# Kernel tuning notes

Measured on AMD Instinct MI355X. Metric: run time of the kernel, lower is better.

Reference implementation:

```python
import jax, jax.numpy as jnp
import numpy as np

B, S, H = 8, 2048, 1024

def setup_inputs() -> dict:
    key = jax.random.key(0)
    ks = jax.random.split(key, 7)
    s = 1.0 / np.sqrt(H)
    return {
        "x": jax.random.normal(ks[0], (B, S, H), dtype=jnp.float32),
        "Wq": jax.random.normal(ks[1], (H, H), dtype=jnp.float32) * s,
        "bq": jnp.zeros((H,), dtype=jnp.float32),
        "Wk": jax.random.normal(ks[2], (H, H), dtype=jnp.float32) * s,
        "bk": jnp.zeros((H,), dtype=jnp.float32),
        "Wv": jax.random.normal(ks[3], (H, H), dtype=jnp.float32) * s,
        "bv": jnp.zeros((H,), dtype=jnp.float32),
    }

def reference(x, Wq, bq, Wk, bk, Wv, bv):
    # Q,K,V: [B,S,H]
    Q = x @ Wq + bq
    K = x @ Wk + bk
    V = x @ Wv + bv
    scale = 1.0 / jnp.sqrt(jnp.asarray(K.shape[-1], dtype=Q.dtype))
    scores = jnp.einsum("bqh,bkh->bqk", Q, K) * scale  # [B,S,S]
    attn = jax.nn.softmax(scores, axis=-1)
    return jnp.einsum("bqk,bkh->bqh", attn, V)
```

## Files before the change

### kernel.cpp

```cpp
#include <hip/hip_runtime.h>
#include <stdint.h>

#define BD 8
#define SD 2048
#define HD 1024

typedef __bf16 bf16x8 __attribute__((ext_vector_type(8)));
typedef float f32x4 __attribute__((ext_vector_type(4)));
typedef unsigned short u16x8 __attribute__((ext_vector_type(8)));
typedef unsigned short u16x4 __attribute__((ext_vector_type(4)));

typedef const __attribute__((address_space(1))) void* gas_ptr;
typedef __attribute__((address_space(3))) void* las_ptr;

__device__ __forceinline__ void gload16(const void* g, void* l) {
  __builtin_amdgcn_global_load_lds((gas_ptr)g, (las_ptr)l, 16, 0, 0);
}

__device__ __forceinline__ unsigned short f32_to_bf16(float f) {
  union { float f; unsigned u; } v; v.f = f;
  unsigned u = v.u;
  return (unsigned short)((u + 0x7FFFu + ((u >> 16) & 1u)) >> 16);
}
__device__ __forceinline__ float bf16_to_f32(unsigned short h) {
  union { unsigned u; float f; } v; v.u = ((unsigned)h) << 16;
  return v.f;
}

__global__ __launch_bounds__(256) void cast_x_kernel(
    const float* __restrict__ x, unsigned short* __restrict__ xb) {
  size_t i = (size_t)blockIdx.x * 256 + threadIdx.x;
  const float4* xp = (const float4*)x;
  float4 a = xp[2*i], b = xp[2*i + 1];
  float v[8] = {a.x,a.y,a.z,a.w,b.x,b.y,b.z,b.w};
  u16x8 o;
#pragma unroll
  for (int j = 0; j < 8; j++) o[j] = f32_to_bf16(v[j]);
  *(u16x8*)(xb + i*8) = o;
}

__global__ __launch_bounds__(256) void transpose_w_kernel(
    const float* __restrict__ Wq, const float* __restrict__ Wk,
    const float* __restrict__ Wv, unsigned short* __restrict__ wt) {
  __shared__ float tile[32][33];
  const int w = blockIdx.z;
  const float* W = (w == 0) ? Wq : ((w == 1) ? Wk : Wv);
  const int n0 = blockIdx.x * 32, k0 = blockIdx.y * 32;
  const int x = threadIdx.x, y = threadIdx.y;
  for (int j = 0; j < 32; j += 8)
    tile[y + j][x] = W[(size_t)(k0 + y + j) * HD + n0 + x];
  __syncthreads();
  unsigned short* dst = wt + (size_t)w * HD * HD;
  for (int j = 0; j < 32; j += 8)
    dst[(size_t)(n0 + y + j) * HD + k0 + x] = f32_to_bf16(tile[x][y + j]);
}

template<int OUT_MODE>
__global__ __launch_bounds__(512, 2) void gemm256(
    const unsigned short* __restrict__ A, size_t sA,
    const unsigned short* __restrict__ Bt, size_t sB,
    const float* __restrict__ b0, const float* __restrict__ b1,
    const float* __restrict__ b2,
    float* __restrict__ Cf, unsigned short* __restrict__ Cb, size_t sC,
    int M, int N, int K, float alpha)
{
  __shared__ unsigned short As[2 * 256 * 64];
  __shared__ unsigned short Bs[2 * 256 * 64];

  const int gx = gridDim.x, gy = gridDim.y;
  const int nwg = gx * gy * gridDim.z;
  const int flat = blockIdx.x + gx * (blockIdx.y + gy * blockIdx.z);
  const int swz = (flat & 7) * (nwg >> 3) + (flat >> 3);
  const int tz = swz / (gx * gy);
  const int rem = swz - tz * gx * gy;
  const int ty = rem / gx, tx = rem - (rem / gx) * gx;
  const int m0 = ty * 256, n0 = tx * 256;

  A  += (size_t)tz * sA;
  Bt += (size_t)tz * sB;
  const float* bias = (tz == 0) ? b0 : ((tz == 1) ? b1 : b2);

  const int tid = threadIdx.x, lane = tid & 63, w = tid >> 6;
  const int wr = w >> 2, wc = w & 3;
  const int nt = K >> 6;

  const int lrow = lane >> 3;
  const int sslot8 = (((lane & 7) ^ ((lane >> 3) & 7)) << 3);

  const int rA = wr * 128 + (lane & 15);
  const int rB = wc * 64 + (lane & 15);
  const int qq = lane >> 4;
  const int sxor = lane & 7;

#define STAGE_A(t,h) do { \
    const unsigned short* _g = A + (size_t)(m0 + (h)*128 + w*16 + lrow) * K + (size_t)((t)*64 + sslot8); \
    unsigned short* _l = &As[((((t)&1)*256 + (h)*128 + w*16)) * 64]; \
    gload16(_g, _l); gload16(_g + (size_t)8*K, _l + 512); } while(0)
#define STAGE_B(t,h) do { \
    const unsigned short* _g = Bt + (size_t)(n0 + (h)*128 + w*16 + lrow) * K + (size_t)((t)*64 + sslot8); \
    unsigned short* _l = &Bs[((((t)&1)*256 + (h)*128 + w*16)) * 64]; \
    gload16(_g, _l); gload16(_g + (size_t)8*K, _l + 512); } while(0)
#define LDA(buf,m,ks) __builtin_bit_cast(bf16x8, *(const u16x8*)(&As[(buf)*16384 + (rA + (m)*16)*64 + ((((ks)*4 + qq) ^ sxor) << 3)]))
#define LDB(buf,n,ks) __builtin_bit_cast(bf16x8, *(const u16x8*)(&Bs[(buf)*16384 + (rB + (n)*16)*64 + ((((ks)*4 + qq) ^ sxor) << 3)]))
#define MFMA_Q(AV,MBASE,NLO) \
    _Pragma("unroll") for (int _m = 0; _m < 4; _m++) \
    _Pragma("unroll") for (int _n = 0; _n < 2; _n++) \
    _Pragma("unroll") for (int _k = 0; _k < 2; _k++) \
      acc[(MBASE)+_m][(NLO)+_n] = __builtin_amdgcn_mfma_f32_16x16x32_bf16( \
          AV[_m][_k], bv[(NLO)+_n][_k], acc[(MBASE)+_m][(NLO)+_n], 0, 0, 0);

  f32x4 acc[8][4] = {};
  bf16x8 av0[4][2], av1[4][2], bv[4][2];

  STAGE_B(0,0); STAGE_B(0,1); STAGE_A(0,0); STAGE_A(0,1);
  STAGE_B(1,0); STAGE_B(1,1); STAGE_A(1,0);
  asm volatile("s_waitcnt vmcnt(6)" ::: "memory");
  __builtin_amdgcn_s_barrier();

  for (int t = 0; t < nt; ++t) {
    const int cur = t & 1;
#pragma unroll
    for (int n = 0; n < 4; n++) { bv[n][0] = LDB(cur,n,0); bv[n][1] = LDB(cur,n,1); }
#pragma unroll
    for (int m = 0; m < 4; m++) { av0[m][0] = LDA(cur,m,0); av0[m][1] = LDA(cur,m,1); }
    if (t + 1 < nt) STAGE_A(t+1, 1);
    __builtin_amdgcn_s_barrier();
    __builtin_amdgcn_s_setprio(1);
    MFMA_Q(av0, 0, 0);
    __builtin_amdgcn_s_setprio(0);
    __builtin_amdgcn_s_barrier();
#pragma unroll
    for (int m = 0; m < 4; m++) { av1[m][0] = LDA(cur,m+4,0); av1[m][1] = LDA(cur,m+4,1); }
    if (t + 2 < nt) STAGE_B(t+2, 0);
    __builtin_amdgcn_s_barrier();
    __builtin_amdgcn_s_setprio(1);
    MFMA_Q(av0, 0, 2);
    __builtin_amdgcn_s_setprio(0);
    __builtin_amdgcn_s_barrier();
    if (t + 2 < nt) STAGE_B(t+2, 1);
    __builtin_amdgcn_s_barrier();
    __builtin_amdgcn_s_setprio(1);
    MFMA_Q(av1, 4, 0);
    __builtin_amdgcn_s_setprio(0);
    __builtin_amdgcn_s_barrier();
    if (t + 2 < nt) STAGE_A(t+2, 0);
    __builtin_amdgcn_s_barrier();
    __builtin_amdgcn_s_setprio(1);
    MFMA_Q(av1, 4, 2);
    __builtin_amdgcn_s_setprio(0);
    if (t < nt - 2) asm volatile("s_waitcnt vmcnt(6)" ::: "memory");
    else            asm volatile("s_waitcnt vmcnt(0)" ::: "memory");
    __builtin_amdgcn_s_barrier();
  }

  const bool transposed = (OUT_MODE == 2) && (tz == 2);
  if (OUT_MODE == 0) {
    float* Cfz = Cf + (size_t)tz * sC;
#pragma unroll
    for (int n = 0; n < 4; n++) {
      const int col = n0 + wc * 64 + n * 16 + (lane & 15);
      const float bvv = bias ? bias[col] : 0.0f;
#pragma unroll
      for (int m = 0; m < 8; m++) {
        const int row = m0 + wr * 128 + m * 16 + (lane >> 4) * 4;
#pragma unroll
        for (int r = 0; r < 4; r++)
          Cfz[(size_t)(row + r) * N + col] = (acc[m][n][r] + bvv) * alpha;
      }
    }
  } else if (!transposed) {
    unsigned short* Cbz = Cb + (size_t)tz * sC;
    unsigned short* base = (w < 4) ? (As + w * 8192) : (Bs + (w - 4) * 8192);
    float bvv[4];
#pragma unroll
    for (int n = 0; n < 4; n++)
      bvv[n] = bias ? bias[n0 + wc * 64 + n * 16 + (lane & 15)] : 0.0f;
#pragma unroll
    for (int n = 0; n < 4; n++)
#pragma unroll
      for (int m = 0; m < 8; m++)
#pragma unroll
        for (int r = 0; r < 4; r++) {
          const int lr = m * 16 + (lane >> 4) * 4 + r;
          const int lc = n * 16 + (lane & 15);
          base[lr * 64 + ((((lc >> 3) ^ (lr & 7)) << 3) | (lc & 7))] =
              f32_to_bf16((acc[m][n][r] + bvv[n]) * alpha);
        }
#pragma unroll
    for (int i = 0; i < 16; i++) {
      const int lr = i * 8 + (lane >> 3);
      u16x8 vrow = *(const u16x8*)(base + lr * 64 + (((lane & 7) ^ (lr & 7)) << 3));
      *(u16x8*)(Cbz + (size_t)(m0 + wr * 128 + lr) * N
                + (n0 + wc * 64 + (lane & 7) * 8)) = vrow;
    }
  } else {
    unsigned short* Vt = Cb + (size_t)2 * sC;
    unsigned short* Vtb = Vt + (size_t)(m0 >> 11) * (HD * SD);
    const int s0 = (m0 & 2047) + wr * 128;
    const int h0 = n0 + wc * 64;
    unsigned short* base = (w < 4) ? (As + w * 8192) : (Bs + (w - 4) * 8192);
    float bvv[4];
#pragma unroll
    for (int n = 0; n < 4; n++)
      bvv[n] = bias ? bias[h0 + n * 16 + (lane & 15)] : 0.0f;
#pragma unroll
    for (int n = 0; n < 4; n++) {
      const int col = n * 16 + (lane & 15);
      const int x = (col & 7) << 3;
#pragma unroll
      for (int m = 0; m < 8; m++) {
        const int row0 = m * 16 + (lane >> 4) * 4;
        u16x4 pk;
#pragma unroll
        for (int r = 0; r < 4; r++)
          pk[r] = f32_to_bf16((acc[m][n][r] + bvv[n]) * alpha);
        *(u16x4*)(base + col * 128 + (row0 ^ x)) = pk;
      }
    }
#pragma unroll
    for (int i = 0; i < 16; i++) {
      const int c = i * 4 + (lane >> 4);
      const int j = lane & 15;
      u16x8 vrow = *(const u16x8*)(base + c * 128 + ((j * 8) ^ ((c & 7) << 3)));
      *(u16x8*)(Vtb + (size_t)(h0 + c) * SD + s0 + j * 8) = vrow;
    }
  }
#undef STAGE_A
#undef STAGE_B
#undef LDA
#undef LDB
#undef MFMA_Q
}

__global__ __launch_bounds__(256) void softmax_bf16_kernel(
    unsigned short* __restrict__ S) {
  const int row = blockIdx.x;
  unsigned short* sp = S + (size_t)row * SD;
  const int tid = threadIdx.x, lane = tid & 63, w = tid >> 6;
  u16x8 raw = *(const u16x8*)(sp + tid * 8);
  float x[8];
#pragma unroll
  for (int j = 0; j < 8; j++) x[j] = bf16_to_f32(raw[j]);
  float m = x[0];
#pragma unroll
  for (int j = 1; j < 8; j++) m = fmaxf(m, x[j]);
#pragma unroll
  for (int off = 32; off >= 1; off >>= 1) m = fmaxf(m, __shfl_xor(m, off));
  __shared__ float redm[4];
  if (lane == 0) redm[w] = m;
  __syncthreads();
  m = fmaxf(fmaxf(redm[0], redm[1]), fmaxf(redm[2], redm[3]));
  float e[8]; float s = 0.0f;
#pragma unroll
  for (int j = 0; j < 8; j++) { e[j] = __expf(x[j] - m); s += e[j]; }
#pragma unroll
  for (int off = 32; off >= 1; off >>= 1) s += __shfl_xor(s, off);
  __shared__ float reds[4];
  if (lane == 0) reds[w] = s;
  __syncthreads();
  s = reds[0] + reds[1] + reds[2] + reds[3];
  const float inv = 1.0f / s;
  u16x8 o;
#pragma unroll
  for (int j = 0; j < 8; j++) o[j] = f32_to_bf16(e[j] * inv);
  *(u16x8*)(sp + tid * 8) = o;
}

extern "C" void kernel_launch(void* const* d_in, const int* in_sizes, int n_in,
                              void* d_out, int out_size, void* d_ws, size_t ws_size,
                              hipStream_t stream) {
  const float* x  = (const float*)d_in[0];
  const float* Wq = (const float*)d_in[1];
  const float* bq = (const float*)d_in[2];
  const float* Wk = (const float*)d_in[3];
  const float* bk = (const float*)d_in[4];
  const float* Wv = (const float*)d_in[5];
  const float* bv = (const float*)d_in[6];
  float* out = (float*)d_out;
  char* ws = (char*)d_ws;
  const size_t MB = 1024 * 1024;
  const float scale = 0.03125f;
  const size_t BH = (size_t)SD * HD;
  const size_t SS = (size_t)SD * SD;

  unsigned short* wt = (unsigned short*)(ws + 0);
  unsigned short* Qb = (unsigned short*)(ws + 6 * MB);
  unsigned short* Kb = (unsigned short*)(ws + 38 * MB);
  unsigned short* Vt = (unsigned short*)(ws + 70 * MB);
  unsigned short* xb = (unsigned short*)(ws + 102 * MB);
  unsigned short* Pb = (unsigned short*)(ws + 102 * MB);

  int G;
  if      (ws_size >= 166 * MB) G = 8;
  else if (ws_size >= 134 * MB) G = 4;
  else if (ws_size >= 118 * MB) G = 2;
  else                          G = 1;

  transpose_w_kernel<<<dim3(32, 32, 3), dim3(32, 8), 0, stream>>>(Wq, Wk, Wv, wt);
  cast_x_kernel<<<8192, 256, 0, stream>>>(x, xb);

  gemm256<2><<<dim3(HD/256, (BD*SD)/256, 3), 512, 0, stream>>>(
      xb, 0, wt, (size_t)HD*HD, bq, bk, bv,
      nullptr, Qb, (size_t)16*MB, BD*SD, HD, HD, 1.0f);

  const int ngroups = BD / G;
  for (int g = 0; g < ngroups; g++) {
    gemm256<1><<<dim3(SD/256, SD/256, G), 512, 0, stream>>>(
        Qb + (size_t)g*G*BH, BH, Kb + (size_t)g*G*BH, BH,
        nullptr, nullptr, nullptr, nullptr, Pb, SS, SD, SD, HD, scale);
    softmax_bf16_kernel<<<G*SD, 256, 0, stream>>>(Pb);
    gemm256<0><<<dim3(HD/256, SD/256, G), 512, 0, stream>>>(
        Pb, SS, Vt + (size_t)g*G*BH, BH, nullptr, nullptr, nullptr,
        out + (size_t)g*G*BH, nullptr, BH, SD, HD, SD, 1.0f);
  }
}
```

Before: 295.1 us.

## Fuse fp32-to-bf16 cast of x into QKV projection GEMM A-tile staging

Removes the separate cast_x kernel and its bf16 intermediate buffer. The QKV GEMM now loads fp32 x directly through registers, converts it to bf16 and writes it into swizzled LDS, while B still uses async global-to-LDS loads. This saves one kernel launch and a write and read of the bf16 copy of x. In exchange, fp32 A reads are re-done by each of the 12 N/z tiles (4 N tiles times Q, K and V), doubling A-read bytes per tile. The synchronous register staging with lgkmcnt waits may also hurt the GEMM pipeline's overlap.

```diff
diff --git a/kernel.cpp b/kernel.cpp
--- a/kernel.cpp
+++ b/kernel.cpp
@@ -25,18 +25,6 @@
 __device__ __forceinline__ float bf16_to_f32(unsigned short h) {
   union { unsigned u; float f; } v; v.u = ((unsigned)h) << 16;
   return v.f;
-}
-
-__global__ __launch_bounds__(256) void cast_x_kernel(
-    const float* __restrict__ x, unsigned short* __restrict__ xb) {
-  size_t i = (size_t)blockIdx.x * 256 + threadIdx.x;
-  const float4* xp = (const float4*)x;
-  float4 a = xp[2*i], b = xp[2*i + 1];
-  float v[8] = {a.x,a.y,a.z,a.w,b.x,b.y,b.z,b.w};
-  u16x8 o;
-#pragma unroll
-  for (int j = 0; j < 8; j++) o[j] = f32_to_bf16(v[j]);
-  *(u16x8*)(xb + i*8) = o;
 }
 
 __global__ __launch_bounds__(256) void transpose_w_kernel(
@@ -55,9 +43,10 @@
     dst[(size_t)(n0 + y + j) * HD + k0 + x] = f32_to_bf16(tile[x][y + j]);
 }
 
-template<int OUT_MODE>
+template<int OUT_MODE, int A_F32>
 __global__ __launch_bounds__(512, 2) void gemm256(
     const unsigned short* __restrict__ A, size_t sA,
+    const float* __restrict__ Af,
     const unsigned short* __restrict__ Bt, size_t sB,
     const float* __restrict__ b0, const float* __restrict__ b1,
     const float* __restrict__ b2,
@@ -96,6 +85,19 @@
     const unsigned short* _g = A + (size_t)(m0 + (h)*128 + w*16 + lrow) * K + (size_t)((t)*64 + sslot8); \
     unsigned short* _l = &As[((((t)&1)*256 + (h)*128 + w*16)) * 64]; \
     gload16(_g, _l); gload16(_g + (size_t)8*K, _l + 512); } while(0)
+#define STAGE_AF(t,h) do { \
+    const int _r = (h)*128 + w*16 + lrow; \
+    const float* _g = Af + (size_t)(m0 + _r) * K + (size_t)(t)*64 + ((lane & 7) * 8); \
+    float4 _a0 = *(const float4*)(_g),          _a1 = *(const float4*)(_g + 4); \
+    float4 _b0 = *(const float4*)(_g + 8*(size_t)K), _b1 = *(const float4*)(_g + 8*(size_t)K + 4); \
+    u16x8 _o0, _o1; \
+    float _v0[8] = {_a0.x,_a0.y,_a0.z,_a0.w,_a1.x,_a1.y,_a1.z,_a1.w}; \
+    float _v1[8] = {_b0.x,_b0.y,_b0.z,_b0.w,_b1.x,_b1.y,_b1.z,_b1.w}; \
+    _Pragma("unroll") for (int _j = 0; _j < 8; _j++) { \
+      _o0[_j] = __builtin_bit_cast(unsigned short, (__bf16)_v0[_j]); \
+      _o1[_j] = __builtin_bit_cast(unsigned short, (__bf16)_v1[_j]); } \
+    unsigned short* _l = &As[((((t)&1)*256 + _r) * 64) + (((lane & 7) ^ (lrow & 7)) * 8)]; \
+    *(u16x8*)_l = _o0; *(u16x8*)(_l + 512) = _o1; } while(0)
 #define STAGE_B(t,h) do { \
     const unsigned short* _g = Bt + (size_t)(n0 + (h)*128 + w*16 + lrow) * K + (size_t)((t)*64 + sslot8); \
     unsigned short* _l = &Bs[((((t)&1)*256 + (h)*128 + w*16)) * 64]; \
@@ -112,9 +114,17 @@
   f32x4 acc[8][4] = {};
   bf16x8 av0[4][2], av1[4][2], bv[4][2];
 
-  STAGE_B(0,0); STAGE_B(0,1); STAGE_A(0,0); STAGE_A(0,1);
-  STAGE_B(1,0); STAGE_B(1,1); STAGE_A(1,0);
-  asm volatile("s_waitcnt vmcnt(6)" ::: "memory");
+  STAGE_B(0,0); STAGE_B(0,1);
+  if constexpr (A_F32) { STAGE_AF(0,0); STAGE_AF(0,1); }
+  else                 { STAGE_A(0,0);  STAGE_A(0,1);  }
+  STAGE_B(1,0); STAGE_B(1,1);
+  if constexpr (A_F32) STAGE_AF(1,0); else STAGE_A(1,0);
+  if constexpr (A_F32) {
+    asm volatile("s_waitcnt vmcnt(4)" ::: "memory");
+    asm volatile("s_waitcnt lgkmcnt(0)" ::: "memory");
+  } else {
+    asm volatile("s_waitcnt vmcnt(6)" ::: "memory");
+  }
   __builtin_amdgcn_s_barrier();
 
   for (int t = 0; t < nt; ++t) {
@@ -123,7 +133,7 @@
     for (int n = 0; n < 4; n++) { bv[n][0] = LDB(cur,n,0); bv[n][1] = LDB(cur,n,1); }
 #pragma unroll
     for (int m = 0; m < 4; m++) { av0[m][0] = LDA(cur,m,0); av0[m][1] = LDA(cur,m,1); }
-    if (t + 1 < nt) STAGE_A(t+1, 1);
+    if (t + 1 < nt) { if constexpr (A_F32) STAGE_AF(t+1, 1); else STAGE_A(t+1, 1); }
     __builtin_amdgcn_s_barrier();
     __builtin_amdgcn_s_setprio(1);
     MFMA_Q(av0, 0, 0);
@@ -143,13 +153,19 @@
     MFMA_Q(av1, 4, 0);
     __builtin_amdgcn_s_setprio(0);
     __builtin_amdgcn_s_barrier();
-    if (t + 2 < nt) STAGE_A(t+2, 0);
+    if (t + 2 < nt) { if constexpr (A_F32) STAGE_AF(t+2, 0); else STAGE_A(t+2, 0); }
     __builtin_amdgcn_s_barrier();
     __builtin_amdgcn_s_setprio(1);
     MFMA_Q(av1, 4, 2);
     __builtin_amdgcn_s_setprio(0);
-    if (t < nt - 2) asm volatile("s_waitcnt vmcnt(6)" ::: "memory");
-    else            asm volatile("s_waitcnt vmcnt(0)" ::: "memory");
+    if constexpr (A_F32) {
+      if (t < nt - 2) asm volatile("s_waitcnt vmcnt(4)" ::: "memory");
+      else            asm volatile("s_waitcnt vmcnt(0)" ::: "memory");
+      asm volatile("s_waitcnt lgkmcnt(0)" ::: "memory");
+    } else {
+      if (t < nt - 2) asm volatile("s_waitcnt vmcnt(6)" ::: "memory");
+      else            asm volatile("s_waitcnt vmcnt(0)" ::: "memory");
+    }
     __builtin_amdgcn_s_barrier();
   }
 
@@ -226,6 +242,7 @@
     }
   }
 #undef STAGE_A
+#undef STAGE_AF
 #undef STAGE_B
 #undef LDA
 #undef LDB
@@ -287,7 +304,6 @@
   unsigned short* Qb = (unsigned short*)(ws + 6 * MB);
   unsigned short* Kb = (unsigned short*)(ws + 38 * MB);
   unsigned short* Vt = (unsigned short*)(ws + 70 * MB);
-  unsigned short* xb = (unsigned short*)(ws + 102 * MB);
   unsigned short* Pb = (unsigned short*)(ws + 102 * MB);
 
   int G;
@@ -297,20 +313,19 @@
   else                          G = 1;
 
   transpose_w_kernel<<<dim3(32, 32, 3), dim3(32, 8), 0, stream>>>(Wq, Wk, Wv, wt);
-  cast_x_kernel<<<8192, 256, 0, stream>>>(x, xb);
-
-  gemm256<2><<<dim3(HD/256, (BD*SD)/256, 3), 512, 0, stream>>>(
-      xb, 0, wt, (size_t)HD*HD, bq, bk, bv,
+
+  gemm256<2,1><<<dim3(HD/256, (BD*SD)/256, 3), 512, 0, stream>>>(
+      nullptr, 0, x, wt, (size_t)HD*HD, bq, bk, bv,
       nullptr, Qb, (size_t)16*MB, BD*SD, HD, HD, 1.0f);
 
   const int ngroups = BD / G;
   for (int g = 0; g < ngroups; g++) {
-    gemm256<1><<<dim3(SD/256, SD/256, G), 512, 0, stream>>>(
-        Qb + (size_t)g*G*BH, BH, Kb + (size_t)g*G*BH, BH,
+    gemm256<1,0><<<dim3(SD/256, SD/256, G), 512, 0, stream>>>(
+        Qb + (size_t)g*G*BH, BH, nullptr, Kb + (size_t)g*G*BH, BH,
         nullptr, nullptr, nullptr, nullptr, Pb, SS, SD, SD, HD, scale);
     softmax_bf16_kernel<<<G*SD, 256, 0, stream>>>(Pb);
-    gemm256<0><<<dim3(HD/256, SD/256, G), 512, 0, stream>>>(
-        Pb, SS, Vt + (size_t)g*G*BH, BH, nullptr, nullptr, nullptr,
+    gemm256<0,0><<<dim3(HD/256, SD/256, G), 512, 0, stream>>>(
+        Pb, SS, nullptr, Vt + (size_t)g*G*BH, BH, nullptr, nullptr, nullptr,
         out + (size_t)g*G*BH, nullptr, BH, SD, HD, SD, 1.0f);
   }
 }
```

Result: slower. 327.7 us (+11.0%).
